# Kernel optimization log

Hardware: AMD Instinct MI355X
Metric: run time of the kernel (lower is better)

The kernel has to match this reference:

```python
import jax, jax.numpy as jnp
import numpy as np

EPS = 1e-5
B, T, IN, EMD, CELL, OUT = 32768, 128, 2, 128, 128, 5


def batchnorm(x, gamma, beta):
    # BatchNorm1d in training mode: biased batch stats over batch dim
    mu = jnp.mean(x, axis=0, keepdims=True)
    var = jnp.var(x, axis=0, keepdims=True)
    return gamma * (x - mu) * jax.lax.rsqrt(var + EPS) + beta


def setup_inputs() -> dict:
    key = jax.random.key(0)
    ks = jax.random.split(key, 8)
    s = 0.05
    return {
        "inputs": jax.random.normal(ks[0], (B, T, IN), dtype=jnp.float32),
        # input embedding MLP: Linear(2,128) + BN + ReLU
        "w_emb": jax.random.normal(ks[1], (EMD, IN), dtype=jnp.float32) * s,
        "b_emb": jnp.zeros((EMD,), dtype=jnp.float32),
        "gamma1": jnp.ones((EMD,), dtype=jnp.float32),
        "beta1": jnp.zeros((EMD,), dtype=jnp.float32),
        # LSTMCell(emd_size, cell_size): gate order i,f,g,o
        "w_ih": jax.random.normal(ks[2], (4 * CELL, EMD), dtype=jnp.float32) * s,
        "w_hh": jax.random.normal(ks[3], (4 * CELL, CELL), dtype=jnp.float32) * s,
        "b_ih": jnp.zeros((4 * CELL,), dtype=jnp.float32),
        "b_hh": jnp.zeros((4 * CELL,), dtype=jnp.float32),
        # output MLP: Linear(128,5) + BN + ReLU
        "w_out": jax.random.normal(ks[4], (OUT, CELL), dtype=jnp.float32) * s,
        "b_out": jnp.zeros((OUT,), dtype=jnp.float32),
        "gamma2": jnp.ones((OUT,), dtype=jnp.float32),
        "beta2": jnp.zeros((OUT,), dtype=jnp.float32),
    }


def reference(inputs, w_emb, b_emb, gamma1, beta1, w_ih, w_hh, b_ih, b_hh,
              w_out, b_out, gamma2, beta2):
    x_tbd = jnp.transpose(inputs, (1, 0, 2))  # [T, B, IN]

    def step(carry, x_t):
        h, c = carry
        # input embedding MLP (train-mode BN + ReLU)
        e = jax.nn.relu(batchnorm(x_t @ w_emb.T + b_emb, gamma1, beta1))
        # LSTM cell
        gates = e @ w_ih.T + b_ih + h @ w_hh.T + b_hh  # [B, 4*CELL]
        i, f, g, o = jnp.split(gates, 4, axis=-1)
        c_new = jax.nn.sigmoid(f) * c + jax.nn.sigmoid(i) * jnp.tanh(g)
        h_new = jax.nn.sigmoid(o) * jnp.tanh(c_new)
        # output MLP (train-mode BN + ReLU)
        y = jax.nn.relu(batchnorm(h_new @ w_out.T + b_out, gamma2, beta2))
        return (h_new, c_new), y

    h0 = jnp.zeros((inputs.shape[0], CELL), dtype=inputs.dtype)
    c0 = jnp.zeros((inputs.shape[0], CELL), dtype=inputs.dtype)
    _, ys = jax.lax.scan(step, (h0, c0), x_tbd)  # ys: [T, B, OUT]
    return jnp.transpose(ys, (1, 0, 2))  # [B, T, OUT]
```

## Files before the change

### kernel.cpp

```cpp
#include <hip/hip_runtime.h>
#include <math.h>

#define B_    32768
#define T_    128
#define OUT_  5
#define EPS_  1e-5f

typedef float f32x4 __attribute__((ext_vector_type(4)));
typedef __bf16 bfrag __attribute__((ext_vector_type(8)));
typedef unsigned short ushort_t;

#define WS_WC2   0
#define WS_GB    67584
#define WS_A0    68112
#define WS_A1    84496
#define WS_C     100880
#define WS_IST   117264
#define WS_ZST   117904

__device__ __forceinline__ ushort_t f2bf(float f) {
  unsigned u = __float_as_uint(f);
  u += 0x7FFFu + ((u >> 16) & 1u);
  return (ushort_t)(u >> 16);
}
__device__ __forceinline__ unsigned cvtpk(float lo, float hi) {
  unsigned r;
  asm("v_cvt_pk_bf16_f32 %0, %1, %2" : "=v"(r) : "v"(lo), "v"(hi));
  return r;
}
__device__ __forceinline__ float fsig(float x) {
  return __builtin_amdgcn_rcpf(1.f + __expf(-x));
}
__device__ __forceinline__ float ftanh(float x) {
  return 1.f - 2.f * __builtin_amdgcn_rcpf(1.f + __expf(2.f * x));
}

__global__ void k_istats(const float* __restrict__ x, float* __restrict__ istats) {
  const int tid = threadIdx.x;
  const int t = tid >> 1;
  const int i = tid & 1;
  const long b0 = (long)blockIdx.x * 64;
  float s_v = 0.f, s_vv = 0.f, s_cross = 0.f;
  for (int s = 0; s < 64; ++s) {
    float v = x[(b0 + s) * 256 + tid];
    float p = __shfl_xor(v, 1);
    s_v += v; s_vv += v * v; s_cross += v * p;
  }
  float* st = istats + t * 5;
  if (i == 0) {
    atomicAdd(st + 0, s_v); atomicAdd(st + 2, s_vv); atomicAdd(st + 4, s_cross);
  } else {
    atomicAdd(st + 1, s_v); atomicAdd(st + 3, s_vv);
  }
}

__global__ void k_prep_w(const float* __restrict__ w_ih, const float* __restrict__ w_hh,
                         const float* __restrict__ w_out, const float* __restrict__ b_ih,
                         const float* __restrict__ b_hh, const float* __restrict__ b_out,
                         ushort_t* __restrict__ Wc2, float* __restrict__ gbias) {
  int idx = blockIdx.x * 256 + threadIdx.x;
  int e = idx & 7;
  int lm = (idx >> 3) & 15;
  int lq = (idx >> 7) & 3;
  int ks = (idx >> 9) & 7;
  int T = idx >> 12;
  int k = ks * 32 + lq * 8 + e;
  float v;
  if (T < 32) {
    int g = T * 16 + lm;
    v = (k < 128) ? w_ih[g * 128 + k] : w_hh[g * 128 + (k - 128)];
  } else {
    v = (k >= 128 && lm < OUT_) ? w_out[lm * 128 + (k - 128)] : 0.f;
  }
  Wc2[idx] = f2bf(v);
  if (idx < 528) {
    float bv = (idx < 512) ? b_ih[idx] + b_hh[idx]
                           : (idx < 517 ? b_out[idx - 512] : 0.f);
    gbias[idx] = bv;
  }
}

__global__ void k_coef(const float* __restrict__ istats, const float* __restrict__ w_emb,
                       const float* __restrict__ b_emb, const float* __restrict__ gamma1,
                       const float* __restrict__ beta1, float* __restrict__ A0,
                       float* __restrict__ A1, float* __restrict__ C) {
  int idx = blockIdx.x * 256 + threadIdx.x;
  int t = idx >> 7, f = idx & 127;
  const float* st = istats + t * 5;
  const float invB = 1.f / (float)B_;
  float m0 = st[0] * invB, m1 = st[1] * invB;
  float v00 = st[2] * invB - m0 * m0;
  float v11 = st[3] * invB - m1 * m1;
  float c01 = st[4] * invB - m0 * m1;
  float w0 = w_emb[f * 2 + 0], w1 = w_emb[f * 2 + 1];
  float mu = m0 * w0 + m1 * w1 + b_emb[f];
  float var = w0 * w0 * v00 + w1 * w1 * v11 + 2.f * w0 * w1 * c01;
  float alpha = gamma1[f] * rsqrtf(var + EPS_);
  A0[t * 128 + f] = alpha * w0;
  A1[t * 128 + f] = alpha * w1;
  C[t * 128 + f] = alpha * (b_emb[f] - mu) + beta1[f];
}

#define GATE_TILE(MT, PB)                                                         \
  {                                                                               \
    const ushort_t* arow_ = &Abuf[(MT) * 16 + lm][0];                             \
    _Pragma("unroll")                                                             \
    for (int i = 0; i < 4; ++i) {                                                 \
      f32x4 v_ = {bias_g[i], bias_g[i], bias_g[i], bias_g[i]};                    \
      acc[PB][i] = v_;                                                            \
    }                                                                             \
    _Pragma("unroll")                                                             \
    for (int ks = 0; ks < 8; ++ks) {                                              \
      const int col_ = (ks < 4 ? pe + ks * 32 : ph + (ks - 4) * 32) + lq * 8;     \
      const bfrag Af_ = __builtin_bit_cast(bfrag, *(const uint4*)(arow_ + col_)); \
      _Pragma("unroll")                                                           \
      for (int i = 0; i < 4; ++i)                                                 \
        acc[PB][i] = __builtin_amdgcn_mfma_f32_16x16x32_bf16(                     \
            Af_, __builtin_bit_cast(bfrag, wreg[i][ks]), acc[PB][i], 0, 0, 0);    \
    }                                                                             \
    if ((MT) == w && t > 0) {                                                     \
      const ushort_t* hrow_ = &Abuf[w * 16 + lm][0];                              \
      f32x4 z_ = {bias_z, bias_z, bias_z, bias_z};                                \
      _Pragma("unroll")                                                           \
      for (int i = 0; i < 4; ++i) {                                               \
        const bfrag Ah_ = __builtin_bit_cast(                                     \
            bfrag, *(const uint4*)(hrow_ + ph + i * 32 + lq * 8));                \
        z_ = __builtin_amdgcn_mfma_f32_16x16x32_bf16(                             \
            Ah_, __builtin_bit_cast(bfrag, wzr[i]), z_, 0, 0, 0);                 \
      }                                                                           \
      zac = z_;                                                                   \
    }                                                                             \
  }

#define EW_TILE(MT, PB)                                                           \
  {                                                                               \
    if ((MT) == w && t > 0) {                                                     \
      float sz_ = 0.f, sq_ = 0.f;                                                 \
      _Pragma("unroll")                                                           \
      for (int r = 0; r < 4; ++r) {                                               \
        const float zv_ = zac[r];                                                 \
        sz_ += zv_; sq_ += zv_ * zv_;                                             \
      }                                                                           \
      sz_ += __shfl_xor(sz_, 16); sz_ += __shfl_xor(sz_, 32);                     \
      sq_ += __shfl_xor(sq_, 16); sq_ += __shfl_xor(sq_, 32);                     \
      if (lq == 0 && lm < OUT_) { zredS[p][w][lm] = sz_; zredQ[p][w][lm] = sq_; } \
      if (((t - 1) & 1) == 0) {                                                   \
        zh0 = zac;                                                                \
      } else {                                                                    \
        zh1 = zac;                                                                \
        if (lm < OUT_) {                                                          \
          const size_t sb0_ = (size_t)(b0 + (w << 4) + lq * 4) * (T_ * OUT_) +    \
                              (size_t)(t - 2) * OUT_ + lm;                        \
          _Pragma("unroll")                                                       \
          for (int r = 0; r < 4; ++r) {                                           \
            const size_t sb_ = sb0_ + (size_t)r * (T_ * OUT_);                    \
            out[sb_] = zh0[r];                                                    \
            out[sb_ + OUT_] = zh1[r];                                             \
          }                                                                       \
        }                                                                         \
      }                                                                           \
    }                                                                             \
    if (t < T_) {                                                                 \
      _Pragma("unroll")                                                           \
      for (int r = 0; r < 4; ++r) {                                               \
        const float gi_ = acc[PB][0][r], gf_ = acc[PB][1][r];                     \
        const float gg_ = acc[PB][2][r], go_ = acc[PB][3][r];                     \
        const float ig_ = fsig(gi_), fg_ = fsig(gf_);                             \
        const float g2_ = ftanh(gg_), og_ = fsig(go_);                            \
        const float cn_ = fmaf(fg_, cst[MT][r], ig_ * g2_);                       \
        cst[MT][r] = cn_;                                                         \
        const float h_ = og_ * ftanh(cn_);                                        \
        Abuf[(MT) * 16 + lq * 4 + r][hw + (w << 4) + lm] =                        \
            (ushort_t)cvtpk(h_, h_);                                              \
      }                                                                           \
    }                                                                             \
  }

__global__ __launch_bounds__(512, 2) void k_lstm(
    const float* __restrict__ x, const ushort_t* __restrict__ Wc2,
    const float* __restrict__ gbias, const float* __restrict__ A0,
    const float* __restrict__ A1, const float* __restrict__ Cc,
    float* __restrict__ out, float* __restrict__ zstats) {
  __shared__ __align__(16) ushort_t Abuf[128][520];
  __shared__ float zredS[2][8][5], zredQ[2][8][5];

  const int tid = threadIdx.x;
  const int w = tid >> 6;
  const int l = tid & 63;
  const int lm = l & 15;
  const int lq = l >> 4;
  const long b0 = (long)blockIdx.x * 128;

  const uint4* W4 = (const uint4*)Wc2;

  uint4 wreg[4][8];
#pragma unroll
  for (int i = 0; i < 4; ++i)
#pragma unroll
    for (int ks = 0; ks < 8; ++ks)
      wreg[i][ks] = W4[((w + 8 * i) * 8 + ks) * 64 + l];
  uint4 wzr[4];
#pragma unroll
  for (int i = 0; i < 4; ++i) wzr[i] = W4[(32 * 8 + 4 + i) * 64 + l];

  float bias_g[4];
#pragma unroll
  for (int i = 0; i < 4; ++i) bias_g[i] = gbias[(w + 8 * i) * 16 + lm];
  const float bias_z = gbias[512 + lm];

  const int em = (w << 4) + (l >> 2);
  const int ec = l & 3;
  const float2* x2 = (const float2*)x;

  float cst[8][4];
#pragma unroll
  for (int mt = 0; mt < 8; ++mt)
#pragma unroll
    for (int r = 0; r < 4; ++r) cst[mt][r] = 0.f;

  f32x4 zh0 = {0.f, 0.f, 0.f, 0.f}, zh1 = zh0;

  for (int i = tid; i < 128 * 520 / 8; i += 512)
    ((uint4*)&Abuf[0][0])[i] = make_uint4(0u, 0u, 0u, 0u);
  __syncthreads();

  for (int t = 0; t <= T_; ++t) {
    const int p = t & 1;
    const int pe = p * 128;
    const int ph = 256 + (p ^ 1) * 128;
    const int hw = 256 + p * 128;

    if (t < T_) {
      float2 xv = x2[(size_t)(b0 + em) * 128 + t];
      const float* A0t = A0 + t * 128;
      const float* A1t = A1 + t * 128;
      const float* Cct = Cc + t * 128;
#pragma unroll
      for (int pp = 0; pp < 4; ++pp) {
        const int f0 = pp * 32 + ec * 8;
        const f32x4 a0l = *(const f32x4*)(A0t + f0);
        const f32x4 a0h = *(const f32x4*)(A0t + f0 + 4);
        const f32x4 a1l = *(const f32x4*)(A1t + f0);
        const f32x4 a1h = *(const f32x4*)(A1t + f0 + 4);
        const f32x4 ccl = *(const f32x4*)(Cct + f0);
        const f32x4 cch = *(const f32x4*)(Cct + f0 + 4);
        unsigned pk[4];
#pragma unroll
        for (int j = 0; j < 2; ++j) {
          float e0 = fmaf(xv.x, a0l[2 * j],     fmaf(xv.y, a1l[2 * j],     ccl[2 * j]));
          float e1 = fmaf(xv.x, a0l[2 * j + 1], fmaf(xv.y, a1l[2 * j + 1], ccl[2 * j + 1]));
          pk[j] = cvtpk(fmaxf(e0, 0.f), fmaxf(e1, 0.f));
          float e2 = fmaf(xv.x, a0h[2 * j],     fmaf(xv.y, a1h[2 * j],     cch[2 * j]));
          float e3 = fmaf(xv.x, a0h[2 * j + 1], fmaf(xv.y, a1h[2 * j + 1], cch[2 * j + 1]));
          pk[2 + j] = cvtpk(fmaxf(e2, 0.f), fmaxf(e3, 0.f));
        }
        *(uint4*)&Abuf[em][pe + f0] = make_uint4(pk[0], pk[1], pk[2], pk[3]);
      }
    }
    __syncthreads();

    if (t >= 2 && tid < 10) {
      const int o = tid >> 1, kind = tid & 1;
      float s = 0.f;
#pragma unroll
      for (int ww = 0; ww < 8; ++ww)
        s += kind ? zredQ[p ^ 1][ww][o] : zredS[p ^ 1][ww][o];
      atomicAdd(&zstats[(size_t)(t - 2) * 10 + o * 2 + kind], s);
    }

    f32x4 acc[2][4];
    f32x4 zac = {0.f, 0.f, 0.f, 0.f};
    GATE_TILE(0, 0)
#pragma unroll
    for (int mt = 1; mt < 8; ++mt) {
      GATE_TILE(mt, (mt & 1))
      EW_TILE((mt - 1), ((mt - 1) & 1))
    }
    EW_TILE(7, 1)
  }

  __syncthreads();
  if (tid < 10) {
    const int o = tid >> 1, kind = tid & 1;
    float s = 0.f;
#pragma unroll
    for (int ww = 0; ww < 8; ++ww) s += kind ? zredQ[0][ww][o] : zredS[0][ww][o];
    atomicAdd(&zstats[(size_t)(T_ - 1) * 10 + o * 2 + kind], s);
  }
}

__global__ void k_outbn(float* __restrict__ out, const float* __restrict__ zstats,
                        const float* __restrict__ gamma2, const float* __restrict__ beta2) {
  int idx = blockIdx.x * 256 + threadIdx.x;
  int r = idx % 640;
  int t = r / 5, o = r - t * 5;
  float z = out[idx];
  float sum = zstats[t * 10 + o * 2];
  float ss = zstats[t * 10 + o * 2 + 1];
  float mu = sum * (1.f / (float)B_);
  float var = ss * (1.f / (float)B_) - mu * mu;
  float y = gamma2[o] * (z - mu) * rsqrtf(var + EPS_) + beta2[o];
  out[idx] = fmaxf(y, 0.f);
}

extern "C" void kernel_launch(void* const* d_in, const int* in_sizes, int n_in, void* d_out,
                              int out_size, void* d_ws, size_t ws_size, hipStream_t stream) {
  const float* x = (const float*)d_in[0];
  const float* w_emb = (const float*)d_in[1];
  const float* b_emb = (const float*)d_in[2];
  const float* gamma1 = (const float*)d_in[3];
  const float* beta1 = (const float*)d_in[4];
  const float* w_ih = (const float*)d_in[5];
  const float* w_hh = (const float*)d_in[6];
  const float* b_ih = (const float*)d_in[7];
  const float* b_hh = (const float*)d_in[8];
  const float* w_out = (const float*)d_in[9];
  const float* b_out = (const float*)d_in[10];
  const float* gamma2 = (const float*)d_in[11];
  const float* beta2 = (const float*)d_in[12];
  float* out = (float*)d_out;
  float* ws = (float*)d_ws;

  ushort_t* Wc2 = (ushort_t*)(ws + WS_WC2);
  float* gbias = ws + WS_GB;
  float* A0 = ws + WS_A0;
  float* A1 = ws + WS_A1;
  float* C = ws + WS_C;
  float* istats = ws + WS_IST;
  float* zstats = ws + WS_ZST;

  hipMemsetAsync(istats, 0, 640 * sizeof(float), stream);
  hipMemsetAsync(zstats, 0, 1280 * sizeof(float), stream);

  k_istats<<<512, 256, 0, stream>>>(x, istats);
  k_prep_w<<<528, 256, 0, stream>>>(w_ih, w_hh, w_out, b_ih, b_hh, b_out, Wc2, gbias);
  k_coef<<<64, 256, 0, stream>>>(istats, w_emb, b_emb, gamma1, beta1, A0, A1, C);
  k_lstm<<<256, 512, 0, stream>>>(x, Wc2, gbias, A0, A1, C, out, zstats);
  k_outbn<<<(B_ * T_ * OUT_) / 256, 256, 0, stream>>>(out, zstats, gamma2, beta2);
}
```

Before: 1.524 ms.

## Stage embedding coefficients in LDS, prefetch x, and batch transcendental ops

Per-timestep embedding coefficients (A0, A1, Cc) are copied into a double-buffered shared-memory tile every 8 steps instead of being read from global memory on every step. The next step's input x is prefetched after the barrier. The gate nonlinearities are reordered so all exps, then all reciprocals, are issued in batches for more instruction-level parallelism. This costs about 24KB of extra LDS, which may limit occupancy at 2 blocks per CU.

```diff
diff --git a/kernel.cpp b/kernel.cpp
--- a/kernel.cpp
+++ b/kernel.cpp
@@ -27,12 +27,6 @@
   unsigned r;
   asm("v_cvt_pk_bf16_f32 %0, %1, %2" : "=v"(r) : "v"(lo), "v"(hi));
   return r;
-}
-__device__ __forceinline__ float fsig(float x) {
-  return __builtin_amdgcn_rcpf(1.f + __expf(-x));
-}
-__device__ __forceinline__ float ftanh(float x) {
-  return 1.f - 2.f * __builtin_amdgcn_rcpf(1.f + __expf(2.f * x));
 }
 
 __global__ void k_istats(const float* __restrict__ x, float* __restrict__ istats) {
@@ -161,15 +155,33 @@
       }                                                                           \
     }                                                                             \
     if (t < T_) {                                                                 \
-      _Pragma("unroll")                                                           \
-      for (int r = 0; r < 4; ++r) {                                               \
-        const float gi_ = acc[PB][0][r], gf_ = acc[PB][1][r];                     \
-        const float gg_ = acc[PB][2][r], go_ = acc[PB][3][r];                     \
-        const float ig_ = fsig(gi_), fg_ = fsig(gf_);                             \
-        const float g2_ = ftanh(gg_), og_ = fsig(go_);                            \
-        const float cn_ = fmaf(fg_, cst[MT][r], ig_ * g2_);                       \
+      float ei_[4], ef_[4], eg_[4], eo_[4];                                       \
+      _Pragma("unroll")                                                           \
+      for (int r = 0; r < 4; ++r) {                                               \
+        ei_[r] = __expf(-acc[PB][0][r]);                                          \
+        ef_[r] = __expf(-acc[PB][1][r]);                                          \
+        eg_[r] = __expf(2.f * acc[PB][2][r]);                                     \
+        eo_[r] = __expf(-acc[PB][3][r]);                                          \
+      }                                                                           \
+      float ig_[4], fg_[4], tg_[4], og_[4];                                       \
+      _Pragma("unroll")                                                           \
+      for (int r = 0; r < 4; ++r) {                                               \
+        ig_[r] = __builtin_amdgcn_rcpf(1.f + ei_[r]);                             \
+        fg_[r] = __builtin_amdgcn_rcpf(1.f + ef_[r]);                             \
+        tg_[r] = 1.f - 2.f * __builtin_amdgcn_rcpf(1.f + eg_[r]);                 \
+        og_[r] = __builtin_amdgcn_rcpf(1.f + eo_[r]);                             \
+      }                                                                           \
+      float eh_[4];                                                               \
+      _Pragma("unroll")                                                           \
+      for (int r = 0; r < 4; ++r) {                                               \
+        const float cn_ = fmaf(fg_[r], cst[MT][r], ig_[r] * tg_[r]);              \
         cst[MT][r] = cn_;                                                         \
-        const float h_ = og_ * ftanh(cn_);                                        \
+        eh_[r] = __expf(2.f * cn_);                                               \
+      }                                                                           \
+      _Pragma("unroll")                                                           \
+      for (int r = 0; r < 4; ++r) {                                               \
+        const float th_ = 1.f - 2.f * __builtin_amdgcn_rcpf(1.f + eh_[r]);        \
+        const float h_ = og_[r] * th_;                                            \
         Abuf[(MT) * 16 + lq * 4 + r][hw + (w << 4) + lm] =                        \
             (ushort_t)cvtpk(h_, h_);                                              \
       }                                                                           \
@@ -182,6 +194,7 @@
     const float* __restrict__ A1, const float* __restrict__ Cc,
     float* __restrict__ out, float* __restrict__ zstats) {
   __shared__ __align__(16) ushort_t Abuf[128][520];
+  __shared__ __align__(16) float Acoef[2][3][8][128];
   __shared__ float zredS[2][8][5], zredQ[2][8][5];
 
   const int tid = threadIdx.x;
@@ -222,6 +235,14 @@
 
   for (int i = tid; i < 128 * 520 / 8; i += 512)
     ((uint4*)&Abuf[0][0])[i] = make_uint4(0u, 0u, 0u, 0u);
+  {
+    const int off = tid * 4;
+    const float* src = (off < 1024) ? (A0 + off) : (A1 + (off - 1024));
+    *(f32x4*)(&Acoef[0][0][0][0] + off) = *(const f32x4*)src;
+    if (tid < 256)
+      *(f32x4*)(&Acoef[0][0][0][0] + 2048 + tid * 4) = *(const f32x4*)(Cc + tid * 4);
+  }
+  float2 xv_cur = x2[(size_t)(b0 + em) * 128 + 0];
   __syncthreads();
 
   for (int t = 0; t <= T_; ++t) {
@@ -231,33 +252,42 @@
     const int hw = 256 + p * 128;
 
     if (t < T_) {
-      float2 xv = x2[(size_t)(b0 + em) * 128 + t];
-      const float* A0t = A0 + t * 128;
-      const float* A1t = A1 + t * 128;
-      const float* Cct = Cc + t * 128;
+      const float* cf = &Acoef[(t >> 3) & 1][0][t & 7][0];
 #pragma unroll
       for (int pp = 0; pp < 4; ++pp) {
         const int f0 = pp * 32 + ec * 8;
-        const f32x4 a0l = *(const f32x4*)(A0t + f0);
-        const f32x4 a0h = *(const f32x4*)(A0t + f0 + 4);
-        const f32x4 a1l = *(const f32x4*)(A1t + f0);
-        const f32x4 a1h = *(const f32x4*)(A1t + f0 + 4);
-        const f32x4 ccl = *(const f32x4*)(Cct + f0);
-        const f32x4 cch = *(const f32x4*)(Cct + f0 + 4);
+        const f32x4 a0l = *(const f32x4*)(cf + f0);
+        const f32x4 a0h = *(const f32x4*)(cf + f0 + 4);
+        const f32x4 a1l = *(const f32x4*)(cf + 1024 + f0);
+        const f32x4 a1h = *(const f32x4*)(cf + 1024 + f0 + 4);
+        const f32x4 ccl = *(const f32x4*)(cf + 2048 + f0);
+        const f32x4 cch = *(const f32x4*)(cf + 2048 + f0 + 4);
         unsigned pk[4];
 #pragma unroll
         for (int j = 0; j < 2; ++j) {
-          float e0 = fmaf(xv.x, a0l[2 * j],     fmaf(xv.y, a1l[2 * j],     ccl[2 * j]));
-          float e1 = fmaf(xv.x, a0l[2 * j + 1], fmaf(xv.y, a1l[2 * j + 1], ccl[2 * j + 1]));
+          float e0 = fmaf(xv_cur.x, a0l[2 * j],     fmaf(xv_cur.y, a1l[2 * j],     ccl[2 * j]));
+          float e1 = fmaf(xv_cur.x, a0l[2 * j + 1], fmaf(xv_cur.y, a1l[2 * j + 1], ccl[2 * j + 1]));
           pk[j] = cvtpk(fmaxf(e0, 0.f), fmaxf(e1, 0.f));
-          float e2 = fmaf(xv.x, a0h[2 * j],     fmaf(xv.y, a1h[2 * j],     cch[2 * j]));
-          float e3 = fmaf(xv.x, a0h[2 * j + 1], fmaf(xv.y, a1h[2 * j + 1], cch[2 * j + 1]));
+          float e2 = fmaf(xv_cur.x, a0h[2 * j],     fmaf(xv_cur.y, a1h[2 * j],     cch[2 * j]));
+          float e3 = fmaf(xv_cur.x, a0h[2 * j + 1], fmaf(xv_cur.y, a1h[2 * j + 1], cch[2 * j + 1]));
           pk[2 + j] = cvtpk(fmaxf(e2, 0.f), fmaxf(e3, 0.f));
         }
         *(uint4*)&Abuf[em][pe + f0] = make_uint4(pk[0], pk[1], pk[2], pk[3]);
       }
+      if ((t & 7) == 7 && t + 1 < T_) {
+        const int t1 = t + 1;
+        float* dst = &Acoef[(t1 >> 3) & 1][0][0][0];
+        const int off = tid * 4;
+        const float* src = (off < 1024) ? (A0 + t1 * 128 + off)
+                                        : (A1 + t1 * 128 + (off - 1024));
+        *(f32x4*)(dst + off) = *(const f32x4*)src;
+        if (tid < 256)
+          *(f32x4*)(dst + 2048 + tid * 4) = *(const f32x4*)(Cc + t1 * 128 + tid * 4);
+      }
     }
     __syncthreads();
+
+    if (t + 1 < T_) xv_cur = x2[(size_t)(b0 + em) * 128 + (t + 1)];
 
     if (t >= 2 && tid < 10) {
       const int o = tid >> 1, kind = tid & 1;
```

New measurement: 1.481 ms. 2.8% less time.
